# Kernel optimization log

Measured on AMD Instinct MI355X. Metric: run time of the kernel, lower is better.

Reference implementation:

```python
import jax, jax.numpy as jnp
import numpy as np

HIDDEN = 1024
HEADS = 16
D_K = HIDDEN // HEADS
NEG_INF = -jnp.inf


def setup_inputs() -> dict:
    key = jax.random.key(0)
    ks = jax.random.split(key, 9)
    N, S = 4, 2048
    scale = 1.0 / np.sqrt(HIDDEN)
    x = jax.random.normal(ks[0], (N, S, HIDDEN), dtype=jnp.float32)
    attn_mask = jnp.ones((N, S), dtype=jnp.int32)
    Wq = jax.random.normal(ks[1], (HIDDEN, HIDDEN), dtype=jnp.float32) * scale
    bq = jnp.zeros((HIDDEN,), dtype=jnp.float32)
    Wk = jax.random.normal(ks[2], (HIDDEN, HIDDEN), dtype=jnp.float32) * scale
    bk = jnp.zeros((HIDDEN,), dtype=jnp.float32)
    Wv = jax.random.normal(ks[3], (HIDDEN, HIDDEN), dtype=jnp.float32) * scale
    bv = jnp.zeros((HIDDEN,), dtype=jnp.float32)
    Wp = jax.random.normal(ks[4], (HIDDEN, HIDDEN), dtype=jnp.float32) * scale
    bp = jnp.zeros((HIDDEN,), dtype=jnp.float32)
    return {"x": x, "attn_mask": attn_mask, "Wq": Wq, "bq": bq,
            "Wk": Wk, "bk": bk, "Wv": Wv, "bv": bv, "Wp": Wp, "bp": bp}


def reference(x, attn_mask, Wq, bq, Wk, bk, Wv, bv, Wp, bp):
    N, S, _ = x.shape
    H, dk = HEADS, D_K
    # torch nn.Linear: y = x @ W.T + b
    q = (x @ Wq.T + bq).reshape(N, S, H, dk).transpose(0, 2, 1, 3)  # (N,H,S,dk)
    k = (x @ Wk.T + bk).reshape(N, S, H, dk).transpose(0, 2, 1, 3)
    v = (x @ Wv.T + bv).reshape(N, S, H, dk).transpose(0, 2, 1, 3)
    attn = jnp.einsum('nhqd,nhkd->nhqk', q, k) / jnp.sqrt(jnp.float32(dk))
    mask = attn_mask.reshape(N, 1, 1, S)
    attn = jnp.where(mask == 0, NEG_INF, attn)
    attn = jax.nn.softmax(attn, axis=-1)
    # dropout is identity in eval mode
    y = jnp.einsum('nhqk,nhkd->nhqd', attn, v)  # (N,H,S,dk)
    y = y.transpose(0, 2, 1, 3).reshape(N, S, H * dk)
    return y @ Wp.T + bp
```

## Files before the change

kernel.cpp:

```cpp
#include <hip/hip_runtime.h>

typedef unsigned short u16;
typedef unsigned int u32;
typedef unsigned long long u64;
typedef __attribute__((ext_vector_type(8))) short bf16x8;
typedef __attribute__((ext_vector_type(4))) short bf16x4;
typedef __attribute__((ext_vector_type(4))) float f32x4;
typedef __attribute__((ext_vector_type(2))) unsigned int u32x2;

#define AS1(p) ((const __attribute__((address_space(1))) void*)(p))
#define AS3(p) ((__attribute__((address_space(3))) void*)(p))

__device__ __forceinline__ u16 f2bf(float f) {
    u32 u = __float_as_uint(f);
    u += 0x7fff + ((u >> 16) & 1);
    return (u16)(u >> 16);
}
__device__ __forceinline__ u32 pack2bf(float lo, float hi) {
    u32 a = __float_as_uint(lo) + 0x8000u;
    u32 b = __float_as_uint(hi) + 0x8000u;
    return __builtin_amdgcn_perm(b, a, 0x07060302);
}

__device__ __forceinline__ void async16(const u16* g, u16* l) {
    __builtin_amdgcn_global_load_lds(AS1(g), AS3(l), 16, 0, 0);
}

__global__ __launch_bounds__(256) void cvt_kernel(const float* __restrict__ src,
                                                  u16* __restrict__ dst, int n) {
    int idx = (blockIdx.x * 256 + threadIdx.x) * 8;
    if (idx >= n) return;
    float4 a = *(const float4*)(src + idx);
    float4 b = *(const float4*)(src + idx + 4);
    uint4 o;
    o.x = (u32)f2bf(a.x) | ((u32)f2bf(a.y) << 16);
    o.y = (u32)f2bf(a.z) | ((u32)f2bf(a.w) << 16);
    o.z = (u32)f2bf(b.x) | ((u32)f2bf(b.y) << 16);
    o.w = (u32)f2bf(b.z) | ((u32)f2bf(b.w) << 16);
    *(uint4*)(dst + idx) = o;
}

__global__ __launch_bounds__(256) void cvt4_kernel(
    const float* __restrict__ s0, const float* __restrict__ s1,
    const float* __restrict__ s2, const float* __restrict__ s3,
    u16* __restrict__ d0, u16* __restrict__ d1,
    u16* __restrict__ d2, u16* __restrict__ d3) {
    const float* s; u16* d;
    switch (blockIdx.y) {
        case 0:  s = s0; d = d0; break;
        case 1:  s = s1; d = d1; break;
        case 2:  s = s2; d = d2; break;
        default: s = s3; d = d3; break;
    }
    int idx = (blockIdx.x * 256 + threadIdx.x) * 8;
    float4 a = *(const float4*)(s + idx);
    float4 b = *(const float4*)(s + idx + 4);
    uint4 o;
    o.x = (u32)f2bf(a.x) | ((u32)f2bf(a.y) << 16);
    o.y = (u32)f2bf(a.z) | ((u32)f2bf(a.w) << 16);
    o.z = (u32)f2bf(b.x) | ((u32)f2bf(b.y) << 16);
    o.w = (u32)f2bf(b.z) | ((u32)f2bf(b.w) << 16);
    *(uint4*)(d + idx) = o;
}

__global__ __launch_bounds__(256, 2) void gemm_bt(
    const u16* __restrict__ A,
    const u16* __restrict__ Wa, const u16* __restrict__ Wb, const u16* __restrict__ Wc,
    const float* __restrict__ ba, const float* __restrict__ bb, const float* __restrict__ bc,
    void* oa, void* ob_, void* oc, int mode)
{
    constexpr int K = 1024;
    __shared__ u16 smem[128 * 132];
    u16* At = smem;
    u16* Wt = smem + 4096;

    const int tid = threadIdx.x;
    const int lane = tid & 63, wv = tid >> 6;
    const int l15 = lane & 15, quad = lane >> 4;
    const int wr = wv >> 1, wc = wv & 1;

    const int L = blockIdx.x + (blockIdx.y << 3) + (blockIdx.z << 9);
    const int g = L & 7;
    const int j = L >> 3;
    const int z = j >> 6;
    const int r = j & 63;
    const int m0 = ((g << 3) + (r & 7)) * 128;
    const int n0 = (r >> 3) * 128;

    const u16* W = (z == 0) ? Wa : ((z == 1) ? Wb : Wc);
    const float* bs = (z == 0) ? ba : ((z == 1) ? bb : bc);
    void* out = (z == 0) ? oa : ((z == 1) ? ob_ : oc);
    const bool swap_ = (mode == 1) || (z < 2);

    f32x4 acc[4][4];
#pragma unroll
    for (int i = 0; i < 4; ++i)
#pragma unroll
        for (int j2 = 0; j2 < 4; ++j2) acc[i][j2] = (f32x4)0.f;

    const int call0 = wv * 2;
    for (int kk = 0; kk < K; kk += 32) {
#pragma unroll
        for (int jj = 0; jj < 2; ++jj) {
            int c = (call0 + jj) * 64 + lane;
            int row = c >> 2;
            int ko = ((c & 3) ^ (row & 3)) * 8;
            async16(A + (size_t)(m0 + row) * K + kk + ko, &At[(call0 + jj) * 512 + lane * 8]);
            async16(W + (size_t)(n0 + row) * K + kk + ko, &Wt[(call0 + jj) * 512 + lane * 8]);
        }
        __syncthreads();

        bf16x8 af[4], wf[4];
#pragma unroll
        for (int t = 0; t < 4; ++t) {
            int rowa = wr * 64 + t * 16 + l15;
            af[t] = *(const bf16x8*)&At[rowa * 32 + ((quad ^ (rowa & 3)) * 8)];
            int rowb = wc * 64 + t * 16 + l15;
            wf[t] = *(const bf16x8*)&Wt[rowb * 32 + ((quad ^ (rowb & 3)) * 8)];
        }
        if (swap_) {
#pragma unroll
            for (int rt = 0; rt < 4; ++rt)
#pragma unroll
                for (int ct = 0; ct < 4; ++ct)
                    acc[rt][ct] = __builtin_amdgcn_mfma_f32_16x16x32_bf16(wf[ct], af[rt], acc[rt][ct], 0, 0, 0);
        } else {
#pragma unroll
            for (int rt = 0; rt < 4; ++rt)
#pragma unroll
                for (int ct = 0; ct < 4; ++ct)
                    acc[rt][ct] = __builtin_amdgcn_mfma_f32_16x16x32_bf16(af[rt], wf[ct], acc[rt][ct], 0, 0, 0);
        }
        __syncthreads();
    }

    if (mode == 1) {
#pragma unroll
        for (int rt = 0; rt < 4; ++rt)
#pragma unroll
            for (int ct = 0; ct < 4; ++ct) {
                int m_ = m0 + wr * 64 + rt * 16 + l15;
                int ob = n0 + wc * 64 + ct * 16 + quad * 4;
                float4 b4 = *(const float4*)&bs[ob];
                float4 v;
                v.x = acc[rt][ct][0] + b4.x;
                v.y = acc[rt][ct][1] + b4.y;
                v.z = acc[rt][ct][2] + b4.z;
                v.w = acc[rt][ct][3] + b4.w;
                *(float4*)((float*)out + (size_t)m_ * 1024 + ob) = v;
            }
        return;
    }

    const int n = m0 >> 11, s0 = m0 & 2047;
    if (z < 2) {
        const float qs = (z == 0) ? 0.18033688011112042f : 1.0f;
#pragma unroll
        for (int rt = 0; rt < 4; ++rt)
#pragma unroll
            for (int ct = 0; ct < 4; ++ct) {
                int ml = wr * 64 + rt * 16 + l15;
                int ol = wc * 64 + ct * 16 + quad * 4;
                float4 b4 = *(const float4*)&bs[n0 + ol];
                float v0 = (acc[rt][ct][0] + b4.x) * qs;
                float v1 = (acc[rt][ct][1] + b4.y) * qs;
                float v2 = (acc[rt][ct][2] + b4.z) * qs;
                float v3 = (acc[rt][ct][3] + b4.w) * qs;
                u32x2 pv = { pack2bf(v0, v1), pack2bf(v2, v3) };
                *(u32x2*)&smem[ml * 132 + ol] = pv;
            }
        __syncthreads();
        const int h0 = n0 >> 6;
#pragma unroll
        for (int p = 0; p < 8; ++p) {
            int hh = p >> 2, qq = p & 3;
            int m = qq * 32 + (tid >> 3), d = (tid & 7) * 8;
            bf16x8 vv = *(const bf16x8*)&smem[m * 132 + hh * 64 + d];
            u16* dst = (u16*)out + ((size_t)((n * 16 + h0 + hh) * 2048 + s0 + m)) * 64 + d;
            *(bf16x8*)dst = vv;
        }
    } else {
#pragma unroll
        for (int rt = 0; rt < 4; ++rt)
#pragma unroll
            for (int ct = 0; ct < 4; ++ct) {
                int ol = wc * 64 + ct * 16 + l15;
                int ml = wr * 64 + rt * 16 + quad * 4;
                float b = bs[n0 + ol];
                float v0 = acc[rt][ct][0] + b;
                float v1 = acc[rt][ct][1] + b;
                float v2 = acc[rt][ct][2] + b;
                float v3 = acc[rt][ct][3] + b;
                u32x2 pv = { pack2bf(v0, v1), pack2bf(v2, v3) };
                *(u32x2*)&smem[ol * 132 + ml] = pv;
            }
        __syncthreads();
#pragma unroll
        for (int p = 0; p < 8; ++p) {
            int o = p * 16 + (tid >> 4), ms = (tid & 15) * 8;
            bf16x8 vv = *(const bf16x8*)&smem[o * 132 + ms];
            int og = n0 + o;
            int h = og >> 6, d = og & 63;
            u16* dst = (u16*)out + ((size_t)((n * 16 + h) * 64 + d)) * 2048 + s0 + ms;
            *(bf16x8*)dst = vv;
        }
    }
}

__global__ __launch_bounds__(256) void attn_kernel(
    const u16* __restrict__ Q, const u16* __restrict__ K_,
    const u16* __restrict__ VT, const int* __restrict__ mask,
    u16* __restrict__ Y)
{
    constexpr int S = 2048, DK = 64, STR = 72;
    __shared__ u16 Kt[64 * STR];
    __shared__ u16 Vt[64 * STR];
    __shared__ u16 Pq[8][16 * STR];
    __shared__ int mtile[64];

    const int tid = threadIdx.x;
    const int lane = tid & 63, w = tid >> 6;
    const int l15 = lane & 15, quad = lane >> 4;
    const int nh = blockIdx.y;
    const int n = nh >> 4, h = nh & 15;
    const int qbase = blockIdx.x * 128;

    const u16* Qh = Q + (size_t)nh * S * DK;
    const u16* Kh = K_ + (size_t)nh * S * DK;
    const u16* Vh = VT + (size_t)nh * DK * S;

    bf16x8 qf[2][2];
#pragma unroll
    for (int nt = 0; nt < 2; ++nt)
#pragma unroll
        for (int st = 0; st < 2; ++st)
            qf[nt][st] = *(const bf16x8*)(Qh + (size_t)(qbase + w * 32 + nt * 16 + l15) * DK + st * 32 + quad * 8);

    f32x4 o[4][2];
#pragma unroll
    for (int dt = 0; dt < 4; ++dt)
#pragma unroll
        for (int nt = 0; nt < 2; ++nt) o[dt][nt] = (f32x4)0.f;
    float lsum[2] = {0.f, 0.f};

    const int r0 = tid >> 3, c8 = (tid & 7) * 8;
    bf16x8 rk0 = *(const bf16x8*)(Kh + (size_t)r0 * 64 + c8);
    bf16x8 rk1 = *(const bf16x8*)(Kh + (size_t)(r0 + 32) * 64 + c8);
    bf16x8 rv0 = *(const bf16x8*)(Vh + (size_t)r0 * S + c8);
    bf16x8 rv1 = *(const bf16x8*)(Vh + (size_t)(r0 + 32) * S + c8);
    int mreg = 0;
    if (tid < 64) mreg = mask[n * S + tid];

    for (int it = 0; it < 32; ++it) {
        *(bf16x8*)&Kt[r0 * STR + c8] = rk0;
        *(bf16x8*)&Kt[(r0 + 32) * STR + c8] = rk1;
        *(bf16x8*)&Vt[r0 * STR + c8] = rv0;
        *(bf16x8*)&Vt[(r0 + 32) * STR + c8] = rv1;
        if (tid < 64) mtile[tid] = mreg;
        __syncthreads();

        const int kkn = ((it + 1) << 6) & (S - 1);
        rk0 = *(const bf16x8*)(Kh + (size_t)(kkn + r0) * 64 + c8);
        rk1 = *(const bf16x8*)(Kh + (size_t)(kkn + r0 + 32) * 64 + c8);
        rv0 = *(const bf16x8*)(Vh + (size_t)r0 * S + kkn + c8);
        rv1 = *(const bf16x8*)(Vh + (size_t)(r0 + 32) * S + kkn + c8);
        if (tid < 64) mreg = mask[n * S + kkn + tid];

        f32x4 sacc[4][2];
#pragma unroll
        for (int jt = 0; jt < 4; ++jt)
#pragma unroll
            for (int nt = 0; nt < 2; ++nt) sacc[jt][nt] = (f32x4)0.f;
#pragma unroll
        for (int st = 0; st < 2; ++st)
#pragma unroll
            for (int jt = 0; jt < 4; ++jt) {
                bf16x8 kf = *(const bf16x8*)&Kt[(jt * 16 + l15) * STR + st * 32 + quad * 8];
                sacc[jt][0] = __builtin_amdgcn_mfma_f32_16x16x32_bf16(kf, qf[0][st], sacc[jt][0], 0, 0, 0);
                sacc[jt][1] = __builtin_amdgcn_mfma_f32_16x16x32_bf16(kf, qf[1][st], sacc[jt][1], 0, 0, 0);
            }

        const bool fast = (__ballot(mtile[lane] != 0) == ~0ull);
        if (!fast) {
#pragma unroll
            for (int jt = 0; jt < 4; ++jt)
#pragma unroll
                for (int r = 0; r < 4; ++r) {
                    int mv = mtile[jt * 16 + quad * 4 + r];
#pragma unroll
                    for (int nt = 0; nt < 2; ++nt)
                        if (mv == 0) sacc[jt][nt][r] = -1e30f;
                }
        }

#pragma unroll
        for (int nt = 0; nt < 2; ++nt) {
            float ps = 0.f;
#pragma unroll
            for (int jt = 0; jt < 4; ++jt) {
                float e0 = __builtin_amdgcn_exp2f(sacc[jt][nt][0]);
                float e1 = __builtin_amdgcn_exp2f(sacc[jt][nt][1]);
                float e2 = __builtin_amdgcn_exp2f(sacc[jt][nt][2]);
                float e3 = __builtin_amdgcn_exp2f(sacc[jt][nt][3]);
                ps += (e0 + e1) + (e2 + e3);
                u32x2 pv = { pack2bf(e0, e1), pack2bf(e2, e3) };
                *(u32x2*)&Pq[w * 2 + nt][l15 * STR + jt * 16 + quad * 4] = pv;
            }
            lsum[nt] += ps;
        }

#pragma unroll
        for (int kt = 0; kt < 2; ++kt) {
            bf16x8 p0 = *(const bf16x8*)&Pq[w * 2 + 0][l15 * STR + kt * 32 + quad * 8];
            bf16x8 p1 = *(const bf16x8*)&Pq[w * 2 + 1][l15 * STR + kt * 32 + quad * 8];
#pragma unroll
            for (int dt = 0; dt < 4; ++dt) {
                bf16x8 vf = *(const bf16x8*)&Vt[(dt * 16 + l15) * STR + kt * 32 + quad * 8];
                o[dt][0] = __builtin_amdgcn_mfma_f32_16x16x32_bf16(vf, p0, o[dt][0], 0, 0, 0);
                o[dt][1] = __builtin_amdgcn_mfma_f32_16x16x32_bf16(vf, p1, o[dt][1], 0, 0, 0);
            }
        }
        __syncthreads();
    }

#pragma unroll
    for (int nt = 0; nt < 2; ++nt) {
        float ls = lsum[nt];
        ls += __shfl_xor(ls, 16);
        ls += __shfl_xor(ls, 32);
        float rl = (ls > 0.f) ? 1.f / ls : 0.f;
        int qi = qbase + w * 32 + nt * 16 + l15;
#pragma unroll
        for (int dt = 0; dt < 4; ++dt) {
            u32x2 pv = { pack2bf(o[dt][nt][0] * rl, o[dt][nt][1] * rl),
                         pack2bf(o[dt][nt][2] * rl, o[dt][nt][3] * rl) };
            size_t base = ((size_t)(n * 2048 + qi)) * 1024 + h * 64 + dt * 16 + quad * 4;
            *(u32x2*)(Y + base) = pv;
        }
    }
}

extern "C" void kernel_launch(void* const* d_in, const int* in_sizes, int n_in,
                              void* d_out, int out_size, void* d_ws, size_t ws_size,
                              hipStream_t stream) {
    const float* x  = (const float*)d_in[0];
    const int* mask = (const int*)d_in[1];
    const float* Wq = (const float*)d_in[2];
    const float* bq = (const float*)d_in[3];
    const float* Wk = (const float*)d_in[4];
    const float* bk = (const float*)d_in[5];
    const float* Wv = (const float*)d_in[6];
    const float* bv = (const float*)d_in[7];
    const float* Wp = (const float*)d_in[8];
    const float* bp = (const float*)d_in[9];

    char* ws = (char*)d_ws;
    u16* xb  = (u16*)(ws);
    u16* wqb = (u16*)(ws + (16u << 20));
    u16* wkb = (u16*)(ws + (18u << 20));
    u16* wvb = (u16*)(ws + (20u << 20));
    u16* wpb = (u16*)(ws + (22u << 20));
    u16* Qb  = (u16*)(ws + (24u << 20));
    u16* Kb  = (u16*)(ws + (40u << 20));
    u16* Vb  = (u16*)(ws + (56u << 20));
    u16* Yb  = (u16*)(ws + (72u << 20));

    cvt_kernel<<<4096, 256, 0, stream>>>(x, xb, 8388608);
    cvt4_kernel<<<dim3(512, 4), 256, 0, stream>>>(Wq, Wk, Wv, Wp, wqb, wkb, wvb, wpb);

    gemm_bt<<<dim3(8, 64, 3), 256, 0, stream>>>(xb, wqb, wkb, wvb, bq, bk, bv,
                                                (void*)Qb, (void*)Kb, (void*)Vb, 0);

    attn_kernel<<<dim3(16, 64), 256, 0, stream>>>(Qb, Kb, Vb, mask, Yb);

    gemm_bt<<<dim3(8, 64, 1), 256, 0, stream>>>(Yb, wpb, wpb, wpb, bp, bp, bp,
                                                d_out, d_out, d_out, 1);
}
```

Baseline: 314.3 us.

## Double-buffer K/V tiles and feed P to MFMA from registers

Makes the K, V and mask tiles double-buffered in shared memory so the trailing barrier of each iteration can be dropped, leaving one sync per tile. The probability tile no longer round-trips through shared memory: the exp outputs are packed straight into bf16x4 operands for 16x16x16 MFMAs, which match the accumulator layout of the score MFMA. The mask fast-path check now reads the register value instead of shared memory. In exchange the PV product uses more, smaller MFMA instructions with narrower V loads, and shared memory use grows for the two buffers.

```diff
diff --git a/kernel.cpp b/kernel.cpp
--- a/kernel.cpp
+++ b/kernel.cpp
@@ -213,10 +213,9 @@
     u16* __restrict__ Y)
 {
     constexpr int S = 2048, DK = 64, STR = 72;
-    __shared__ u16 Kt[64 * STR];
-    __shared__ u16 Vt[64 * STR];
-    __shared__ u16 Pq[8][16 * STR];
-    __shared__ int mtile[64];
+    __shared__ u16 Kt[2][64 * STR];
+    __shared__ u16 Vt[2][64 * STR];
+    __shared__ int mtile[2][64];
 
     const int tid = threadIdx.x;
     const int lane = tid & 63, w = tid >> 6;
@@ -252,11 +251,13 @@
     if (tid < 64) mreg = mask[n * S + tid];
 
     for (int it = 0; it < 32; ++it) {
-        *(bf16x8*)&Kt[r0 * STR + c8] = rk0;
-        *(bf16x8*)&Kt[(r0 + 32) * STR + c8] = rk1;
-        *(bf16x8*)&Vt[r0 * STR + c8] = rv0;
-        *(bf16x8*)&Vt[(r0 + 32) * STR + c8] = rv1;
-        if (tid < 64) mtile[tid] = mreg;
+        const int b = it & 1;
+        *(bf16x8*)&Kt[b][r0 * STR + c8] = rk0;
+        *(bf16x8*)&Kt[b][(r0 + 32) * STR + c8] = rk1;
+        *(bf16x8*)&Vt[b][r0 * STR + c8] = rv0;
+        *(bf16x8*)&Vt[b][(r0 + 32) * STR + c8] = rv1;
+        if (tid < 64) mtile[b][tid] = mreg;
+        const int mcur = mreg;
         __syncthreads();
 
         const int kkn = ((it + 1) << 6) & (S - 1);
@@ -275,18 +276,18 @@
         for (int st = 0; st < 2; ++st)
 #pragma unroll
             for (int jt = 0; jt < 4; ++jt) {
-                bf16x8 kf = *(const bf16x8*)&Kt[(jt * 16 + l15) * STR + st * 32 + quad * 8];
+                bf16x8 kf = *(const bf16x8*)&Kt[b][(jt * 16 + l15) * STR + st * 32 + quad * 8];
                 sacc[jt][0] = __builtin_amdgcn_mfma_f32_16x16x32_bf16(kf, qf[0][st], sacc[jt][0], 0, 0, 0);
                 sacc[jt][1] = __builtin_amdgcn_mfma_f32_16x16x32_bf16(kf, qf[1][st], sacc[jt][1], 0, 0, 0);
             }
 
-        const bool fast = (__ballot(mtile[lane] != 0) == ~0ull);
+        const bool fast = (__ballot(mcur != 0) == ~0ull);
         if (!fast) {
 #pragma unroll
             for (int jt = 0; jt < 4; ++jt)
 #pragma unroll
                 for (int r = 0; r < 4; ++r) {
-                    int mv = mtile[jt * 16 + quad * 4 + r];
+                    int mv = mtile[b][jt * 16 + quad * 4 + r];
 #pragma unroll
                     for (int nt = 0; nt < 2; ++nt)
                         if (mv == 0) sacc[jt][nt][r] = -1e30f;
@@ -294,33 +295,31 @@
         }
 
 #pragma unroll
-        for (int nt = 0; nt < 2; ++nt) {
-            float ps = 0.f;
-#pragma unroll
-            for (int jt = 0; jt < 4; ++jt) {
-                float e0 = __builtin_amdgcn_exp2f(sacc[jt][nt][0]);
-                float e1 = __builtin_amdgcn_exp2f(sacc[jt][nt][1]);
-                float e2 = __builtin_amdgcn_exp2f(sacc[jt][nt][2]);
-                float e3 = __builtin_amdgcn_exp2f(sacc[jt][nt][3]);
-                ps += (e0 + e1) + (e2 + e3);
-                u32x2 pv = { pack2bf(e0, e1), pack2bf(e2, e3) };
-                *(u32x2*)&Pq[w * 2 + nt][l15 * STR + jt * 16 + quad * 4] = pv;
-            }
-            lsum[nt] += ps;
-        }
-
-#pragma unroll
-        for (int kt = 0; kt < 2; ++kt) {
-            bf16x8 p0 = *(const bf16x8*)&Pq[w * 2 + 0][l15 * STR + kt * 32 + quad * 8];
-            bf16x8 p1 = *(const bf16x8*)&Pq[w * 2 + 1][l15 * STR + kt * 32 + quad * 8];
+        for (int jt = 0; jt < 4; ++jt) {
+            bf16x4 p0, p1;
+            {
+                float e0 = __builtin_amdgcn_exp2f(sacc[jt][0][0]);
+                float e1 = __builtin_amdgcn_exp2f(sacc[jt][0][1]);
+                float e2 = __builtin_amdgcn_exp2f(sacc[jt][0][2]);
+                float e3 = __builtin_amdgcn_exp2f(sacc[jt][0][3]);
+                lsum[0] += (e0 + e1) + (e2 + e3);
+                p0 = __builtin_bit_cast(bf16x4, (u32x2){pack2bf(e0, e1), pack2bf(e2, e3)});
+            }
+            {
+                float e0 = __builtin_amdgcn_exp2f(sacc[jt][1][0]);
+                float e1 = __builtin_amdgcn_exp2f(sacc[jt][1][1]);
+                float e2 = __builtin_amdgcn_exp2f(sacc[jt][1][2]);
+                float e3 = __builtin_amdgcn_exp2f(sacc[jt][1][3]);
+                lsum[1] += (e0 + e1) + (e2 + e3);
+                p1 = __builtin_bit_cast(bf16x4, (u32x2){pack2bf(e0, e1), pack2bf(e2, e3)});
+            }
 #pragma unroll
             for (int dt = 0; dt < 4; ++dt) {
-                bf16x8 vf = *(const bf16x8*)&Vt[(dt * 16 + l15) * STR + kt * 32 + quad * 8];
-                o[dt][0] = __builtin_amdgcn_mfma_f32_16x16x32_bf16(vf, p0, o[dt][0], 0, 0, 0);
-                o[dt][1] = __builtin_amdgcn_mfma_f32_16x16x32_bf16(vf, p1, o[dt][1], 0, 0, 0);
-            }
-        }
-        __syncthreads();
+                bf16x4 vf = *(const bf16x4*)&Vt[b][(dt * 16 + l15) * STR + jt * 16 + quad * 4];
+                o[dt][0] = __builtin_amdgcn_mfma_f32_16x16x16bf16_1k(vf, p0, o[dt][0], 0, 0, 0);
+                o[dt][1] = __builtin_amdgcn_mfma_f32_16x16x16bf16_1k(vf, p1, o[dt][1], 0, 0, 0);
+            }
+        }
     }
 
 #pragma unroll
```

Result: slower. 321.6 us (+2.3%).
